# Optimization experiments

Hardware: AMD Instinct MI355X
Metric: run time of the kernel (lower is better)

The kernel has to match this reference:

```python
import jax, jax.numpy as jnp
import numpy as np

N, T, D_MODEL, H, DK = 4, 4096, 1024, 16, 64


def setup_inputs() -> dict:
    key = jax.random.key(0)
    ks = jax.random.split(key, 16)
    randn = lambda k, sh: jax.random.normal(k, sh, dtype=jnp.float32)
    # linear weights stored (in, out) so y = x @ W + b (math-equivalent to torch Linear)
    scale = 1.0 / np.sqrt(D_MODEL)
    return {
        "x_k": randn(ks[0], (N, T, D_MODEL)),
        "x_v": randn(ks[1], (N, T, D_MODEL)),
        "x_q": randn(ks[2], (N, T, D_MODEL)),
        "mask": jnp.ones((N, T), dtype=jnp.int32),
        "Wk": randn(ks[3], (D_MODEL, H * DK)) * scale,
        "bk": randn(ks[4], (H * DK,)) * 0.02,
        "Wv": randn(ks[5], (D_MODEL, H * DK)) * scale,
        "bv": randn(ks[6], (H * DK,)) * 0.02,
        "Wq": randn(ks[7], (D_MODEL, H * DK)) * scale,
        "bq": randn(ks[8], (H * DK,)) * 0.02,
        "alpha_w": randn(ks[9], (DK,)),
        "beta_w": randn(ks[10], (DK,)),
        "Wr": randn(ks[11], (DK, DK)) * (1.0 / np.sqrt(DK)),
        "br": randn(ks[12], (DK,)) * 0.02,
        "Wfc": randn(ks[13], (H * DK, D_MODEL)) * scale,
        "bfc": randn(ks[14], (D_MODEL,)) * 0.02,
    }


def _split_heads(x):  # (n, t, h*d) -> (n, h, t, d)
    n, t, _ = x.shape
    return x.reshape(n, t, H, DK).transpose(0, 2, 1, 3)


def reference(x_k, x_v, x_q, mask, Wk, bk, Wv, bv, Wq, bq,
              alpha_w, beta_w, Wr, br, Wfc, bfc):
    scale = DK ** (-0.5)
    k = _split_heads(x_k @ Wk + bk)  # (n, h, t, d)
    v = _split_heads(x_v @ Wv + bv)
    q = _split_heads(x_q @ Wq + bq)

    m = (mask == 0)[:, None, :]  # (n, 1, t) True where masked
    neg_inf = jnp.finfo(q.dtype).min

    # alpha pooling over queries -> global query (n, h, d)
    alpha = jnp.einsum('nhtd,d->nht', q, alpha_w) * scale
    alpha = jnp.where(m, neg_inf, alpha)
    alpha = jax.nn.softmax(alpha, axis=-1)
    global_query = jnp.einsum('nht,nhtd->nhd', alpha, q)

    # p = broadcast(global_query) * k, then beta pooling -> global key
    p = global_query[:, :, None, :] * k  # (n, h, t, d)
    beta = jnp.einsum('nhtd,d->nht', p, beta_w) * scale
    beta = jnp.where(m, neg_inf, beta)
    beta = jax.nn.softmax(beta, axis=-1)
    global_key = jnp.einsum('nht,nhtd->nhd', beta, p)

    u = global_key[:, :, None, :] * v  # (n, h, t, d)
    u_r = u @ Wr + br
    A = u_r + q  # (n, h, t, d)
    A = A.transpose(0, 2, 1, 3).reshape(N, T, H * DK)
    return A @ Wfc + bfc
```

## Files before the change

kernel.cpp:

```cpp
#include <hip/hip_runtime.h>

typedef __bf16 bf16x8 __attribute__((ext_vector_type(8)));
typedef float f32x4 __attribute__((ext_vector_type(4)));
typedef unsigned int u32x4 __attribute__((ext_vector_type(4)));
typedef unsigned short u16x4 __attribute__((ext_vector_type(4)));
typedef unsigned short u16x8 __attribute__((ext_vector_type(8)));

#define SEQ_T 4096
#define DMODEL 1024
#define HEADS 16
#define DKH 64
#define MTOK 16384

#define AS1 __attribute__((address_space(1)))
#define AS3 __attribute__((address_space(3)))

__device__ __forceinline__ unsigned short f2bf(float f) {
  unsigned u = __builtin_bit_cast(unsigned int, f);
  u += 0x7FFFu + ((u >> 16) & 1u);
  return (unsigned short)(u >> 16);
}
__device__ __forceinline__ float bf2f(unsigned short h) {
  unsigned u = ((unsigned)h) << 16;
  return __builtin_bit_cast(float, u);
}
__device__ __forceinline__ void gload16(const unsigned short* g, unsigned short* l) {
  __builtin_amdgcn_global_load_lds((const AS1 unsigned int*)(g),
                                   (AS3 unsigned int*)(l), 16, 0, 0);
}

__global__ void __launch_bounds__(256) k_wtrans(const float* __restrict__ W,
                                                unsigned short* __restrict__ Wt,
                                                int K, int N) {
  __shared__ float tile[32][33];
  int bn = blockIdx.x * 32, bk = blockIdx.y * 32;
  int tx = threadIdx.x, ty = threadIdx.y;
#pragma unroll
  for (int j = 0; j < 32; j += 8)
    tile[ty + j][tx] = W[(size_t)(bk + ty + j) * N + bn + tx];
  __syncthreads();
#pragma unroll
  for (int j = 0; j < 32; j += 8)
    Wt[(size_t)(bn + ty + j) * K + bk + tx] = f2bf(tile[tx][ty + j]);
}

#define BM 256
#define BN 256
#define BK 64

template <int OBF, int SCORE, int AF32>
__global__ void __launch_bounds__(512, 2)
k_gemm(const void* __restrict__ Ain, const unsigned short* __restrict__ Bt,
       const float* __restrict__ bias, void* __restrict__ C,
       const int* __restrict__ mask, const float* __restrict__ swt,
       float* __restrict__ sbuf, int M, int N, int K) {
  __shared__ unsigned short Asb[2][BM * BK];
  __shared__ unsigned short Bsb[2][BN * BK];
  const int tid = threadIdx.x;
  const int lane = tid & 63, wid = tid >> 6;
  const int wr = wid >> 2, wc = wid & 3;
  const int l15 = lane & 15, l4 = lane >> 4;

  const int nwg = gridDim.x * gridDim.y;
  const int flat = blockIdx.x + blockIdx.y * gridDim.x;
  const int rm = (flat & 7) * (nwg >> 3) + (flat >> 3);
  const int bx = rm % gridDim.x, by = rm / gridDim.x;
  const int bm = by * BM, bn = bx * BN;

  const float* Af = (const float*)Ain;
  const unsigned short* Abf = (const unsigned short*)Ain;

  f32x4 acc[8][4];
#pragma unroll
  for (int i = 0; i < 8; ++i)
#pragma unroll
    for (int j = 0; j < 4; ++j)
#pragma unroll
      for (int e = 0; e < 4; ++e) acc[i][j][e] = 0.f;

  const int sgr = lane >> 3;
  const int sgc = (lane & 7) ^ sgr;
  const int r0 = tid >> 3;
  const int c7l = tid & 7;
  const int c7s = c7l ^ (r0 & 7);

  f32x4 alo[4], ahi[4];
  auto loadA32 = [&](int t) {
#pragma unroll
    for (int s = 0; s < 4; ++s) {
      const float* src = Af + (size_t)(bm + r0 + s * 64) * K + t * BK + c7s * 8;
      alo[s] = *(const f32x4*)src;
      ahi[s] = *(const f32x4*)(src + 4);
    }
  };
  auto writeA32 = [&](int t) {
    unsigned short* dst = &Asb[t & 1][0];
#pragma unroll
    for (int s = 0; s < 4; ++s) {
      u16x8 o;
#pragma unroll
      for (int j = 0; j < 4; ++j) {
        o[j] = f2bf(alo[s][j]);
        o[4 + j] = f2bf(ahi[s][j]);
      }
      *(u16x8*)(dst + (r0 + s * 64) * BK + c7l * 8) = o;
    }
  };
  auto stageAbf = [&](int t) {
    unsigned short* dst = &Asb[t & 1][0];
#pragma unroll
    for (int j = 0; j < 4; ++j) {
      int g = wid * 4 + j;
      gload16(Abf + (size_t)(bm + g * 8 + sgr) * K + t * BK + sgc * 8,
              dst + g * 512);
    }
  };
  auto stageB = [&](int t) {
    unsigned short* dst = &Bsb[t & 1][0];
#pragma unroll
    for (int j = 0; j < 4; ++j) {
      int g = wid * 4 + j;
      gload16(Bt + (size_t)(bn + g * 8 + sgr) * K + t * BK + sgc * 8,
              dst + g * 512);
    }
  };

  const int nt = K / BK;
  if (AF32) {
    loadA32(0);
    writeA32(0);
  } else {
    stageAbf(0);
  }
  stageB(0);

  for (int t = 0; t < nt; ++t) {
    asm volatile("s_waitcnt vmcnt(0)" ::: "memory");
    asm volatile("s_waitcnt lgkmcnt(0)" ::: "memory");
    __builtin_amdgcn_s_barrier();
    const bool pf = (t + 1 < nt);
    if (pf) {
      if (AF32) loadA32(t + 1); else stageAbf(t + 1);
      stageB(t + 1);
    }
    const unsigned short* Ab = &Asb[t & 1][0];
    const unsigned short* Bb = &Bsb[t & 1][0];
#pragma unroll
    for (int ks = 0; ks < 2; ++ks) {
      bf16x8 bfr[4];
#pragma unroll
      for (int nf = 0; nf < 4; ++nf) {
        int rowb = wc * 64 + nf * 16 + l15;
        int c7 = (ks * 4 + l4) ^ (rowb & 7);
        bfr[nf] = *(const bf16x8*)(Bb + rowb * BK + c7 * 8);
      }
#pragma unroll
      for (int mh = 0; mh < 2; ++mh) {
        bf16x8 af[4];
#pragma unroll
        for (int i = 0; i < 4; ++i) {
          int rowa = wr * 128 + (mh * 4 + i) * 16 + l15;
          int c7 = (ks * 4 + l4) ^ (rowa & 7);
          af[i] = *(const bf16x8*)(Ab + rowa * BK + c7 * 8);
        }
        __builtin_amdgcn_s_setprio(1);
#pragma unroll
        for (int i = 0; i < 4; ++i)
#pragma unroll
          for (int nf = 0; nf < 4; ++nf)
            acc[mh * 4 + i][nf] = __builtin_amdgcn_mfma_f32_16x16x32_bf16(
                af[i], bfr[nf], acc[mh * 4 + i][nf], 0, 0, 0);
        __builtin_amdgcn_s_setprio(0);
      }
    }
    if (pf && AF32) writeA32(t + 1);
    asm volatile("s_waitcnt lgkmcnt(0)" ::: "memory");
    __builtin_amdgcn_s_barrier();
  }

  const int crow = bm + wr * 128 + l4 * 4;
  const int ccol = bn + wc * 64 + l15;
  float pacc[8][4];
  const float* wrow = nullptr;
  if (SCORE == 1) wrow = swt;
  if (SCORE == 2)
    wrow = swt + ((size_t)((bm >> 12) * HEADS + bx * 4 + wc)) * DKH;
  if (SCORE) {
#pragma unroll
    for (int m = 0; m < 8; ++m)
#pragma unroll
      for (int e = 0; e < 4; ++e) pacc[m][e] = 0.f;
  }

#pragma unroll
  for (int m = 0; m < 8; ++m)
#pragma unroll
    for (int nf = 0; nf < 4; ++nf) {
      int c = ccol + nf * 16;
      float bj = bias[c];
      float wg = SCORE ? wrow[nf * 16 + l15] : 0.f;
#pragma unroll
      for (int e = 0; e < 4; ++e) {
        int r = crow + m * 16 + e;
        float v = acc[m][nf][e] + bj;
        if (SCORE) pacc[m][e] += v * wg;
        if (OBF)
          ((unsigned short*)C)[(size_t)r * N + c] = f2bf(v);
        else
          ((float*)C)[(size_t)r * N + c] = v;
      }
    }

  if (SCORE) {
#pragma unroll
    for (int m = 0; m < 8; ++m)
#pragma unroll
      for (int e = 0; e < 4; ++e) {
        float p = pacc[m][e];
        p += __shfl_xor(p, 1);
        p += __shfl_xor(p, 2);
        p += __shfl_xor(p, 4);
        p += __shfl_xor(p, 8);
        if (l15 == 0) {
          int r = crow + m * 16 + e;
          int t = r & (SEQ_T - 1), n = r >> 12;
          float sc = p * 0.125f;
          if (mask[n * SEQ_T + t] == 0) sc = -3.0e38f;
          sbuf[((size_t)n * HEADS + bx * 4 + wc) * SEQ_T + t] = sc;
        }
      }
  }
}

__global__ void __launch_bounds__(256) k_stat1(const float* __restrict__ s,
                                               float* __restrict__ pmax,
                                               float* __restrict__ psum) {
  __shared__ float red[4];
  const int b = blockIdx.x, tid = threadIdx.x, lane = tid & 63, wid = tid >> 6;
  float v = s[(size_t)b * 256 + tid];
  float m = v;
#pragma unroll
  for (int o = 1; o < 64; o <<= 1) m = fmaxf(m, __shfl_xor(m, o));
  if (lane == 0) red[wid] = m;
  __syncthreads();
  m = fmaxf(fmaxf(red[0], red[1]), fmaxf(red[2], red[3]));
  __syncthreads();
  float e = __expf(v - m);
#pragma unroll
  for (int o = 1; o < 64; o <<= 1) e += __shfl_xor(e, o);
  if (lane == 0) red[wid] = e;
  __syncthreads();
  if (tid == 0) {
    pmax[b] = m;
    psum[b] = red[0] + red[1] + red[2] + red[3];
  }
}

__global__ void __launch_bounds__(64) k_stat2(const float* __restrict__ pmax,
                                              const float* __restrict__ psum,
                                              float* __restrict__ smx,
                                              float* __restrict__ sinv) {
  const int b = blockIdx.x, lane = threadIdx.x;
  float pm = -3.4e38f, ps = 0.f;
  if (lane < 16) {
    pm = pmax[b * 16 + lane];
    ps = psum[b * 16 + lane];
  }
  float gm = pm;
#pragma unroll
  for (int o = 1; o < 16; o <<= 1) gm = fmaxf(gm, __shfl_xor(gm, o));
  float sc = ps * __expf(pm - gm);
#pragma unroll
  for (int o = 1; o < 16; o <<= 1) sc += __shfl_xor(sc, o);
  if (lane == 0) {
    smx[b] = gm;
    sinv[b] = 1.f / sc;
  }
}

__global__ void __launch_bounds__(256) k_wsum(const unsigned short* __restrict__ X,
                                              const float* __restrict__ s,
                                              const float* __restrict__ mxv,
                                              const float* __restrict__ invv,
                                              float* __restrict__ pbuf) {
  __shared__ float part[16][64];
  const int nh = blockIdx.x >> 4, chunk = blockIdx.x & 15;
  const int n = nh >> 4, h = nh & 15;
  const int tid = threadIdx.x, lane = tid & 63, wid = tid >> 6;
  const int tsub = lane >> 4, dl = lane & 15;
  const float mx = mxv[nh], inv = invv[nh];
  const float* sb = s + (size_t)nh * SEQ_T + chunk * 256;
  const size_t base = ((size_t)n * SEQ_T + chunk * 256) * DMODEL + h * DKH + dl * 4;
  f32x4 acc = {0.f, 0.f, 0.f, 0.f};
  for (int t = wid * 4 + tsub; t < 256; t += 16) {
    float w = __expf(sb[t] - mx) * inv;
    u16x4 xv = *(const u16x4*)(X + base + (size_t)t * DMODEL);
    acc[0] += w * bf2f(xv[0]);
    acc[1] += w * bf2f(xv[1]);
    acc[2] += w * bf2f(xv[2]);
    acc[3] += w * bf2f(xv[3]);
  }
  int g = wid * 4 + tsub;
#pragma unroll
  for (int e = 0; e < 4; ++e) part[g][dl * 4 + e] = acc[e];
  __syncthreads();
  if (tid < 64) {
    float v = 0.f;
#pragma unroll
    for (int gg = 0; gg < 16; ++gg) v += part[gg][tid];
    pbuf[(size_t)blockIdx.x * 64 + tid] = v;
  }
}

template <int MODE>
__global__ void __launch_bounds__(64) k_fin(const float* __restrict__ pbuf,
                                            const float* __restrict__ gq,
                                            const float* __restrict__ bw,
                                            float* __restrict__ out,
                                            float* __restrict__ wv) {
  const int nh = blockIdx.x, d = threadIdx.x;
  float v = 0.f;
#pragma unroll
  for (int c = 0; c < 16; ++c) v += pbuf[((size_t)nh * 16 + c) * 64 + d];
  if (MODE == 1) v *= gq[(size_t)nh * 64 + d];
  out[(size_t)nh * 64 + d] = v;
  if (MODE == 0) wv[(size_t)nh * 64 + d] = v * bw[d];
}

__global__ void __launch_bounds__(256) k_wrg(const float* __restrict__ gk,
                                             const float* __restrict__ Wr,
                                             unsigned short* __restrict__ WrgT) {
  const int nh = blockIdx.x, tid = threadIdx.x;
#pragma unroll
  for (int i = 0; i < 16; ++i) {
    int idx = i * 256 + tid;
    int d = idx >> 6, dd = idx & 63;
    WrgT[(size_t)nh * 4096 + idx] = f2bf(gk[nh * 64 + dd] * Wr[dd * 64 + d]);
  }
}

#define ABM 128
#define VLD 72
__global__ void __launch_bounds__(256) k_abuild2(const unsigned short* __restrict__ v,
                                                 const unsigned short* __restrict__ qbf,
                                                 const unsigned short* __restrict__ WrgT,
                                                 const float* __restrict__ br,
                                                 unsigned short* __restrict__ A) {
  __shared__ unsigned short Vs[ABM * VLD];
  __shared__ unsigned short Ws[DKH * VLD];
  const int tid = threadIdx.x, lane = tid & 63, wid = tid >> 6;
  const int nh = blockIdx.y;
  const int n = nh >> 4, h = nh & 15;
  const size_t nt0 = (size_t)n * SEQ_T + (size_t)blockIdx.x * ABM;
  const size_t vbase = nt0 * DMODEL + (size_t)h * DKH;
#pragma unroll
  for (int p = 0; p < 4; ++p) {
    int idx = p * 256 + tid;
    int row = idx >> 3, c = idx & 7;
    *(u32x4*)(Vs + row * VLD + c * 8) =
        *(const u32x4*)(v + vbase + (size_t)row * DMODEL + c * 8);
  }
#pragma unroll
  for (int p = 0; p < 2; ++p) {
    int idx = p * 256 + tid;
    int row = idx >> 3, c = idx & 7;
    *(u32x4*)(Ws + row * VLD + c * 8) =
        *(const u32x4*)(WrgT + (size_t)nh * 4096 + row * 64 + c * 8);
  }
  __syncthreads();
  const int l15 = lane & 15, l4 = lane >> 4;
  f32x4 acc[2][4];
#pragma unroll
  for (int m = 0; m < 2; ++m)
#pragma unroll
    for (int nf = 0; nf < 4; ++nf)
#pragma unroll
      for (int e = 0; e < 4; ++e) acc[m][nf][e] = 0.f;
#pragma unroll
  for (int ks = 0; ks < 2; ++ks) {
    bf16x8 af[2], bfr[4];
#pragma unroll
    for (int m = 0; m < 2; ++m)
      af[m] = *(const bf16x8*)(Vs + (wid * 32 + m * 16 + l15) * VLD + l4 * 8 + ks * 32);
#pragma unroll
    for (int nf = 0; nf < 4; ++nf)
      bfr[nf] = *(const bf16x8*)(Ws + (nf * 16 + l15) * VLD + l4 * 8 + ks * 32);
#pragma unroll
    for (int m = 0; m < 2; ++m)
#pragma unroll
      for (int nf = 0; nf < 4; ++nf)
        acc[m][nf] = __builtin_amdgcn_mfma_f32_16x16x32_bf16(af[m], bfr[nf],
                                                             acc[m][nf], 0, 0, 0);
  }
#pragma unroll
  for (int m = 0; m < 2; ++m)
#pragma unroll
    for (int nf = 0; nf < 4; ++nf) {
      int d = nf * 16 + l15;
      float bj = br[d];
#pragma unroll
      for (int e = 0; e < 4; ++e) {
        int r = wid * 32 + m * 16 + l4 * 4 + e;
        size_t off = vbase + (size_t)r * DMODEL + d;
        float val = acc[m][nf][e] + bj + bf2f(qbf[off]);
        A[off] = f2bf(val);
      }
    }
}

extern "C" void kernel_launch(void* const* d_in, const int* in_sizes, int n_in,
                              void* d_out, int out_size, void* d_ws, size_t ws_size,
                              hipStream_t stream) {
  const float* x_k = (const float*)d_in[0];
  const float* x_v = (const float*)d_in[1];
  const float* x_q = (const float*)d_in[2];
  const int* mask = (const int*)d_in[3];
  const float* Wk = (const float*)d_in[4];
  const float* bk = (const float*)d_in[5];
  const float* Wv = (const float*)d_in[6];
  const float* bv = (const float*)d_in[7];
  const float* Wq = (const float*)d_in[8];
  const float* bq = (const float*)d_in[9];
  const float* alpha_w = (const float*)d_in[10];
  const float* beta_w = (const float*)d_in[11];
  const float* Wr = (const float*)d_in[12];
  const float* br = (const float*)d_in[13];
  const float* Wfc = (const float*)d_in[14];
  const float* bfc = (const float*)d_in[15];

  unsigned short* qbf = (unsigned short*)d_out;

  char* ws = (char*)d_ws;
  const size_t SZ_XBF = (size_t)MTOK * DMODEL * 2;
  unsigned short* kbf = (unsigned short*)(ws);
  unsigned short* vbf = (unsigned short*)(ws + SZ_XBF);
  unsigned short* xst = (unsigned short*)(ws + 2 * SZ_XBF);
  unsigned short* WkT = (unsigned short*)(ws + 3 * SZ_XBF);
  unsigned short* WvT = WkT + (size_t)DMODEL * DMODEL;
  unsigned short* WqT = WvT + (size_t)DMODEL * DMODEL;
  unsigned short* WfT = WqT + (size_t)DMODEL * DMODEL;
  unsigned short* WrgT = WfT + (size_t)DMODEL * DMODEL;
  float* gq = (float*)(WrgT + (size_t)64 * 4096);
  float* gk = gq + 4096;
  float* wvb = gk + 4096;
  float* sbuf = wvb + 4096;
  float* pbuf = sbuf + (size_t)64 * SEQ_T;
  float* pmax = pbuf + 1024 * 64;
  float* psum = pmax + 1024;
  float* smx = psum + 1024;
  float* sinv = smx + 64;

  dim3 tb(32, 8);
  dim3 tg(DMODEL / 32, DMODEL / 32);
  k_wtrans<<<tg, tb, 0, stream>>>(Wq, WqT, DMODEL, DMODEL);
  k_wtrans<<<tg, tb, 0, stream>>>(Wk, WkT, DMODEL, DMODEL);
  k_wtrans<<<tg, tb, 0, stream>>>(Wv, WvT, DMODEL, DMODEL);
  k_wtrans<<<tg, tb, 0, stream>>>(Wfc, WfT, DMODEL, DMODEL);

  dim3 ggrid(DMODEL / BN, MTOK / BM);

  k_gemm<1, 1, 1><<<ggrid, 512, 0, stream>>>(x_q, WqT, bq, (void*)qbf, mask,
                                             alpha_w, sbuf, MTOK, DMODEL, DMODEL);
  k_stat1<<<1024, 256, 0, stream>>>(sbuf, pmax, psum);
  k_stat2<<<64, 64, 0, stream>>>(pmax, psum, smx, sinv);
  k_wsum<<<1024, 256, 0, stream>>>(qbf, sbuf, smx, sinv, pbuf);
  k_fin<0><<<64, 64, 0, stream>>>(pbuf, nullptr, beta_w, gq, wvb);

  k_gemm<1, 2, 1><<<ggrid, 512, 0, stream>>>(x_k, WkT, bk, (void*)kbf, mask,
                                             wvb, sbuf, MTOK, DMODEL, DMODEL);
  k_stat1<<<1024, 256, 0, stream>>>(sbuf, pmax, psum);
  k_stat2<<<64, 64, 0, stream>>>(pmax, psum, smx, sinv);
  k_wsum<<<1024, 256, 0, stream>>>(kbf, sbuf, smx, sinv, pbuf);
  k_fin<1><<<64, 64, 0, stream>>>(pbuf, gq, nullptr, gk, nullptr);

  k_gemm<1, 0, 1><<<ggrid, 512, 0, stream>>>(x_v, WvT, bv, (void*)vbf, nullptr,
                                             nullptr, nullptr, MTOK, DMODEL, DMODEL);

  k_wrg<<<64, 256, 0, stream>>>(gk, Wr, WrgT);
  dim3 agrid(SEQ_T / ABM, 64);
  k_abuild2<<<agrid, 256, 0, stream>>>(vbf, qbf, WrgT, br, xst);

  k_gemm<0, 0, 0><<<ggrid, 512, 0, stream>>>(xst, WfT, bfc, d_out, nullptr,
                                             nullptr, nullptr, MTOK, DMODEL, DMODEL);
}
```

Before: 297.6 us.

## Restructure GEMM into four-phase pipelined schedule with split half-tile LDS staging

Changes the GEMM main loop so each wave owns a 32-row strip across all 256 columns instead of a 128x64 subtile. LDS A and B tiles are split into 128-row halves, and loads are issued per phase, with B prefetched two k-steps ahead and partial vmcnt waits. Each k-step becomes four barrier-separated MFMA phases, so global-to-LDS transfers overlap compute more finely. The intent is to hide load latency and drop the full vmcnt(0) drain per iteration. The cost is more barriers per k-step and more B-fragment LDS reads per wave, since each wave now reads the whole B tile.

```diff
diff --git a/kernel.cpp b/kernel.cpp
--- a/kernel.cpp
+++ b/kernel.cpp
@@ -14,6 +14,7 @@
 
 #define AS1 __attribute__((address_space(1)))
 #define AS3 __attribute__((address_space(3)))
+#define MEMFENCE asm volatile("" ::: "memory")
 
 __device__ __forceinline__ unsigned short f2bf(float f) {
   unsigned u = __builtin_bit_cast(unsigned int, f);
@@ -54,11 +55,10 @@
        const float* __restrict__ bias, void* __restrict__ C,
        const int* __restrict__ mask, const float* __restrict__ swt,
        float* __restrict__ sbuf, int M, int N, int K) {
-  __shared__ unsigned short Asb[2][BM * BK];
-  __shared__ unsigned short Bsb[2][BN * BK];
+  __shared__ unsigned short As[2][2][128 * 64];
+  __shared__ unsigned short Bs[2][2][128 * 64];
   const int tid = threadIdx.x;
   const int lane = tid & 63, wid = tid >> 6;
-  const int wr = wid >> 2, wc = wid & 3;
   const int l15 = lane & 15, l4 = lane >> 4;
 
   const int nwg = gridDim.x * gridDim.y;
@@ -69,141 +69,172 @@
 
   const float* Af = (const float*)Ain;
   const unsigned short* Abf = (const unsigned short*)Ain;
-
-  f32x4 acc[8][4];
-#pragma unroll
-  for (int i = 0; i < 8; ++i)
-#pragma unroll
-    for (int j = 0; j < 4; ++j)
-#pragma unroll
-      for (int e = 0; e < 4; ++e) acc[i][j][e] = 0.f;
+  const int nt = K / BK;
+
+  f32x4 acc[2][16];
+#pragma unroll
+  for (int m = 0; m < 2; ++m)
+#pragma unroll
+    for (int nf = 0; nf < 16; ++nf)
+#pragma unroll
+      for (int e = 0; e < 4; ++e) acc[m][nf][e] = 0.f;
 
   const int sgr = lane >> 3;
   const int sgc = (lane & 7) ^ sgr;
   const int r0 = tid >> 3;
-  const int c7l = tid & 7;
-  const int c7s = c7l ^ (r0 & 7);
-
+  const int c8 = tid & 7;
+  const int cw = c8 ^ (r0 & 7);
   f32x4 alo[4], ahi[4];
-  auto loadA32 = [&](int t) {
+
+  auto stageA = [&](int t, int h) {
+#pragma unroll
+    for (int j = 0; j < 2; ++j) {
+      int g = wid * 2 + j;
+      gload16(Abf + (size_t)(bm + h * 128 + g * 8 + sgr) * K + t * BK + sgc * 8,
+              &As[t & 1][h][g * 512]);
+    }
+  };
+  auto stageB = [&](int t, int h) {
+#pragma unroll
+    for (int j = 0; j < 2; ++j) {
+      int g = wid * 2 + j;
+      gload16(Bt + (size_t)(bn + h * 128 + g * 8 + sgr) * K + t * BK + sgc * 8,
+              &Bs[t & 1][h][g * 512]);
+    }
+  };
+  auto aload = [&](int t) {
 #pragma unroll
     for (int s = 0; s < 4; ++s) {
-      const float* src = Af + (size_t)(bm + r0 + s * 64) * K + t * BK + c7s * 8;
+      const float* src = Af + (size_t)(bm + r0 + s * 64) * K + t * BK + c8 * 8;
       alo[s] = *(const f32x4*)src;
       ahi[s] = *(const f32x4*)(src + 4);
     }
   };
-  auto writeA32 = [&](int t) {
-    unsigned short* dst = &Asb[t & 1][0];
+  auto awrite = [&](int t) {
 #pragma unroll
     for (int s = 0; s < 4; ++s) {
+      int row = r0 + s * 64;
       u16x8 o;
 #pragma unroll
       for (int j = 0; j < 4; ++j) {
         o[j] = f2bf(alo[s][j]);
         o[4 + j] = f2bf(ahi[s][j]);
       }
-      *(u16x8*)(dst + (r0 + s * 64) * BK + c7l * 8) = o;
+      *(u16x8*)(&As[t & 1][row >> 7][(row & 127) * 64 + cw * 8]) = o;
     }
   };
-  auto stageAbf = [&](int t) {
-    unsigned short* dst = &Asb[t & 1][0];
-#pragma unroll
-    for (int j = 0; j < 4; ++j) {
-      int g = wid * 4 + j;
-      gload16(Abf + (size_t)(bm + g * 8 + sgr) * K + t * BK + sgc * 8,
-              dst + g * 512);
-    }
-  };
-  auto stageB = [&](int t) {
-    unsigned short* dst = &Bsb[t & 1][0];
-#pragma unroll
-    for (int j = 0; j < 4; ++j) {
-      int g = wid * 4 + j;
-      gload16(Bt + (size_t)(bn + g * 8 + sgr) * K + t * BK + sgc * 8,
-              dst + g * 512);
-    }
-  };
-
-  const int nt = K / BK;
+
   if (AF32) {
-    loadA32(0);
-    writeA32(0);
+    aload(0);
+    stageB(0, 0);
+    stageB(0, 1);
+    stageB(1, 0);
+    awrite(0);
+    asm volatile("s_waitcnt lgkmcnt(0)" ::: "memory");
+    asm volatile("s_waitcnt vmcnt(4)" ::: "memory");
   } else {
-    stageAbf(0);
-  }
-  stageB(0);
-
+    stageA(0, 0);
+    stageA(0, 1);
+    stageB(0, 0);
+    stageB(0, 1);
+    stageB(1, 0);
+    asm volatile("s_waitcnt vmcnt(4)" ::: "memory");
+  }
+  __builtin_amdgcn_s_barrier();
+  MEMFENCE;
+
+  bf16x8 afr[2][2];
   for (int t = 0; t < nt; ++t) {
-    asm volatile("s_waitcnt vmcnt(0)" ::: "memory");
-    asm volatile("s_waitcnt lgkmcnt(0)" ::: "memory");
-    __builtin_amdgcn_s_barrier();
-    const bool pf = (t + 1 < nt);
-    if (pf) {
-      if (AF32) loadA32(t + 1); else stageAbf(t + 1);
-      stageB(t + 1);
-    }
-    const unsigned short* Ab = &Asb[t & 1][0];
-    const unsigned short* Bb = &Bsb[t & 1][0];
-#pragma unroll
-    for (int ks = 0; ks < 2; ++ks) {
-      bf16x8 bfr[4];
-#pragma unroll
-      for (int nf = 0; nf < 4; ++nf) {
-        int rowb = wc * 64 + nf * 16 + l15;
-        int c7 = (ks * 4 + l4) ^ (rowb & 7);
-        bfr[nf] = *(const bf16x8*)(Bb + rowb * BK + c7 * 8);
+    const int cur = t & 1;
+#pragma unroll
+    for (int p = 0; p < 4; ++p) {
+      if (p == 0) {
+#pragma unroll
+        for (int m = 0; m < 2; ++m)
+#pragma unroll
+          for (int ks = 0; ks < 2; ++ks) {
+            int rh = (wid & 3) * 32 + m * 16 + l15;
+            int c7 = (ks * 4 + l4) ^ (rh & 7);
+            afr[m][ks] = *(const bf16x8*)(&As[cur][wid >> 2][rh * 64 + c7 * 8]);
+          }
       }
-#pragma unroll
-      for (int mh = 0; mh < 2; ++mh) {
-        bf16x8 af[4];
-#pragma unroll
-        for (int i = 0; i < 4; ++i) {
-          int rowa = wr * 128 + (mh * 4 + i) * 16 + l15;
-          int c7 = (ks * 4 + l4) ^ (rowa & 7);
-          af[i] = *(const bf16x8*)(Ab + rowa * BK + c7 * 8);
+      bf16x8 bfr[4][2];
+#pragma unroll
+      for (int nf = 0; nf < 4; ++nf)
+#pragma unroll
+        for (int ks = 0; ks < 2; ++ks) {
+          int rh = (p & 1) * 64 + nf * 16 + l15;
+          int c7 = (ks * 4 + l4) ^ (rh & 7);
+          bfr[nf][ks] = *(const bf16x8*)(&Bs[cur][p >> 1][rh * 64 + c7 * 8]);
         }
-        __builtin_amdgcn_s_setprio(1);
-#pragma unroll
-        for (int i = 0; i < 4; ++i)
-#pragma unroll
-          for (int nf = 0; nf < 4; ++nf)
-            acc[mh * 4 + i][nf] = __builtin_amdgcn_mfma_f32_16x16x32_bf16(
-                af[i], bfr[nf], acc[mh * 4 + i][nf], 0, 0, 0);
-        __builtin_amdgcn_s_setprio(0);
+      if (p == 0) {
+        if (t + 1 < nt) {
+          if (AF32) aload(t + 1);
+          else stageA(t + 1, 0);
+        }
+      } else if (p == 1) {
+        if (!AF32 && t + 1 < nt) stageA(t + 1, 1);
+      } else if (p == 2) {
+        if (t + 2 < nt) stageB(t + 2, 0);
+      } else {
+        if (t + 1 < nt) {
+          stageB(t + 1, 1);
+          if (AF32) awrite(t + 1);
+        }
       }
-    }
-    if (pf && AF32) writeA32(t + 1);
-    asm volatile("s_waitcnt lgkmcnt(0)" ::: "memory");
-    __builtin_amdgcn_s_barrier();
-  }
-
-  const int crow = bm + wr * 128 + l4 * 4;
-  const int ccol = bn + wc * 64 + l15;
-  float pacc[8][4];
-  const float* wrow = nullptr;
-  if (SCORE == 1) wrow = swt;
-  if (SCORE == 2)
-    wrow = swt + ((size_t)((bm >> 12) * HEADS + bx * 4 + wc)) * DKH;
+      if (p == 1) {
+        if (AF32) asm volatile("s_waitcnt vmcnt(8)" ::: "memory");
+        else asm volatile("s_waitcnt vmcnt(4)" ::: "memory");
+      } else if (p == 3) {
+        if (AF32) asm volatile("s_waitcnt lgkmcnt(0)" ::: "memory");
+        asm volatile("s_waitcnt vmcnt(4)" ::: "memory");
+      }
+      MEMFENCE;
+      __builtin_amdgcn_s_barrier();
+      MEMFENCE;
+      __builtin_amdgcn_s_setprio(1);
+#pragma unroll
+      for (int m = 0; m < 2; ++m)
+#pragma unroll
+        for (int nf = 0; nf < 4; ++nf)
+#pragma unroll
+          for (int ks = 0; ks < 2; ++ks)
+            acc[m][p * 4 + nf] = __builtin_amdgcn_mfma_f32_16x16x32_bf16(
+                afr[m][ks], bfr[nf][ks], acc[m][p * 4 + nf], 0, 0, 0);
+      __builtin_amdgcn_s_setprio(0);
+      MEMFENCE;
+      __builtin_amdgcn_s_barrier();
+      MEMFENCE;
+    }
+  }
+
+  const int crow = bm + wid * 32 + l4 * 4;
+  float pacc[2][4][4];
   if (SCORE) {
 #pragma unroll
-    for (int m = 0; m < 8; ++m)
-#pragma unroll
-      for (int e = 0; e < 4; ++e) pacc[m][e] = 0.f;
-  }
-
-#pragma unroll
-  for (int m = 0; m < 8; ++m)
-#pragma unroll
-    for (int nf = 0; nf < 4; ++nf) {
-      int c = ccol + nf * 16;
+    for (int m = 0; m < 2; ++m)
+#pragma unroll
+      for (int hh = 0; hh < 4; ++hh)
+#pragma unroll
+        for (int e = 0; e < 4; ++e) pacc[m][hh][e] = 0.f;
+  }
+
+#pragma unroll
+  for (int m = 0; m < 2; ++m)
+#pragma unroll
+    for (int nf = 0; nf < 16; ++nf) {
+      int c = bn + nf * 16 + l15;
       float bj = bias[c];
-      float wg = SCORE ? wrow[nf * 16 + l15] : 0.f;
+      float wg = 0.f;
+      if (SCORE == 1) wg = swt[(nf & 3) * 16 + l15];
+      if (SCORE == 2)
+        wg = swt[((size_t)((bm >> 12) * HEADS + bx * 4 + (nf >> 2))) * DKH +
+                 (nf & 3) * 16 + l15];
 #pragma unroll
       for (int e = 0; e < 4; ++e) {
         int r = crow + m * 16 + e;
         float v = acc[m][nf][e] + bj;
-        if (SCORE) pacc[m][e] += v * wg;
+        if (SCORE) pacc[m][nf >> 2][e] += v * wg;
         if (OBF)
           ((unsigned short*)C)[(size_t)r * N + c] = f2bf(v);
         else
@@ -213,22 +244,24 @@
 
   if (SCORE) {
 #pragma unroll
-    for (int m = 0; m < 8; ++m)
-#pragma unroll
-      for (int e = 0; e < 4; ++e) {
-        float p = pacc[m][e];
-        p += __shfl_xor(p, 1);
-        p += __shfl_xor(p, 2);
-        p += __shfl_xor(p, 4);
-        p += __shfl_xor(p, 8);
-        if (l15 == 0) {
-          int r = crow + m * 16 + e;
-          int t = r & (SEQ_T - 1), n = r >> 12;
-          float sc = p * 0.125f;
-          if (mask[n * SEQ_T + t] == 0) sc = -3.0e38f;
-          sbuf[((size_t)n * HEADS + bx * 4 + wc) * SEQ_T + t] = sc;
+    for (int m = 0; m < 2; ++m)
+#pragma unroll
+      for (int hh = 0; hh < 4; ++hh)
+#pragma unroll
+        for (int e = 0; e < 4; ++e) {
+          float pv = pacc[m][hh][e];
+          pv += __shfl_xor(pv, 1);
+          pv += __shfl_xor(pv, 2);
+          pv += __shfl_xor(pv, 4);
+          pv += __shfl_xor(pv, 8);
+          if (l15 == 0) {
+            int r = crow + m * 16 + e;
+            int tt = r & (SEQ_T - 1), n = r >> 12;
+            float sc = pv * 0.125f;
+            if (mask[n * SEQ_T + tt] == 0) sc = -3.0e38f;
+            sbuf[((size_t)n * HEADS + bx * 4 + hh) * SEQ_T + tt] = sc;
+          }
         }
-      }
   }
 }
 
```

Result: no change. 296.3 us (-0.4%).

## Restructure GEMM main loop into an eight-phase interleaved ping-pong schedule

Applied to the files above, without the earlier changes.

The GEMM K-loop is rewritten to process two K tiles per iteration in eight phases. Global-to-LDS staging for the next tiles (A load, B load, fp32 A conversion write, vmcnt wait) is spread across the phases between MFMA bursts, instead of being issued in one block at the top of each tile. Shared buffers are split into 128-row halves, and the fp32-A swizzle moves from the global read side to the LDS write side. The aim is finer overlap of memory traffic with MFMA work, at the cost of two barriers per phase and more synchronization overall.

```diff
diff --git a/kernel.cpp b/kernel.cpp
--- a/kernel.cpp
+++ b/kernel.cpp
@@ -14,6 +14,7 @@
 
 #define AS1 __attribute__((address_space(1)))
 #define AS3 __attribute__((address_space(3)))
+#define MEMFENCE asm volatile("" ::: "memory")
 
 __device__ __forceinline__ unsigned short f2bf(float f) {
   unsigned u = __builtin_bit_cast(unsigned int, f);
@@ -54,8 +55,8 @@
        const float* __restrict__ bias, void* __restrict__ C,
        const int* __restrict__ mask, const float* __restrict__ swt,
        float* __restrict__ sbuf, int M, int N, int K) {
-  __shared__ unsigned short Asb[2][BM * BK];
-  __shared__ unsigned short Bsb[2][BN * BK];
+  __shared__ unsigned short As[2][2][128 * 64];
+  __shared__ unsigned short Bs[2][2][128 * 64];
   const int tid = threadIdx.x;
   const int lane = tid & 63, wid = tid >> 6;
   const int wr = wid >> 2, wc = wid & 3;
@@ -69,128 +70,147 @@
 
   const float* Af = (const float*)Ain;
   const unsigned short* Abf = (const unsigned short*)Ain;
+  const int nt = K / BK;
 
   f32x4 acc[8][4];
 #pragma unroll
-  for (int i = 0; i < 8; ++i)
-#pragma unroll
-    for (int j = 0; j < 4; ++j)
-#pragma unroll
-      for (int e = 0; e < 4; ++e) acc[i][j][e] = 0.f;
+  for (int m = 0; m < 8; ++m)
+#pragma unroll
+    for (int nf = 0; nf < 4; ++nf)
+#pragma unroll
+      for (int e = 0; e < 4; ++e) acc[m][nf][e] = 0.f;
 
   const int sgr = lane >> 3;
   const int sgc = (lane & 7) ^ sgr;
   const int r0 = tid >> 3;
-  const int c7l = tid & 7;
-  const int c7s = c7l ^ (r0 & 7);
-
+  const int c8 = tid & 7;
+  const int cw = c8 ^ (r0 & 7);
   f32x4 alo[4], ahi[4];
-  auto loadA32 = [&](int t) {
+
+  auto stageA = [&](int t) {
+#pragma unroll
+    for (int h = 0; h < 2; ++h)
+#pragma unroll
+      for (int j = 0; j < 2; ++j) {
+        int g = wid * 2 + j;
+        gload16(Abf + (size_t)(bm + h * 128 + g * 8 + sgr) * K + t * BK + sgc * 8,
+                &As[t & 1][h][g * 512]);
+      }
+  };
+  auto stageB = [&](int t) {
+#pragma unroll
+    for (int h = 0; h < 2; ++h)
+#pragma unroll
+      for (int j = 0; j < 2; ++j) {
+        int g = wid * 2 + j;
+        gload16(Bt + (size_t)(bn + h * 128 + g * 8 + sgr) * K + t * BK + sgc * 8,
+                &Bs[t & 1][h][g * 512]);
+      }
+  };
+  auto aload = [&](int t) {
 #pragma unroll
     for (int s = 0; s < 4; ++s) {
-      const float* src = Af + (size_t)(bm + r0 + s * 64) * K + t * BK + c7s * 8;
+      const float* src = Af + (size_t)(bm + r0 + s * 64) * K + t * BK + c8 * 8;
       alo[s] = *(const f32x4*)src;
       ahi[s] = *(const f32x4*)(src + 4);
     }
   };
-  auto writeA32 = [&](int t) {
-    unsigned short* dst = &Asb[t & 1][0];
+  auto awrite = [&](int t) {
 #pragma unroll
     for (int s = 0; s < 4; ++s) {
+      int row = r0 + s * 64;
       u16x8 o;
 #pragma unroll
       for (int j = 0; j < 4; ++j) {
         o[j] = f2bf(alo[s][j]);
         o[4 + j] = f2bf(ahi[s][j]);
       }
-      *(u16x8*)(dst + (r0 + s * 64) * BK + c7l * 8) = o;
+      *(u16x8*)(&As[t & 1][row >> 7][(row & 127) * 64 + cw * 8]) = o;
     }
   };
-  auto stageAbf = [&](int t) {
-    unsigned short* dst = &Asb[t & 1][0];
-#pragma unroll
-    for (int j = 0; j < 4; ++j) {
-      int g = wid * 4 + j;
-      gload16(Abf + (size_t)(bm + g * 8 + sgr) * K + t * BK + sgc * 8,
-              dst + g * 512);
+
+  if (AF32) {
+    aload(0);
+    awrite(0);
+  } else {
+    stageA(0);
+  }
+  stageB(0);
+  asm volatile("s_waitcnt vmcnt(0)" ::: "memory");
+  asm volatile("s_waitcnt lgkmcnt(0)" ::: "memory");
+  __builtin_amdgcn_s_barrier();
+  MEMFENCE;
+
+  bf16x8 bfr[4];
+  for (int it = 0; it < nt / 2; ++it) {
+    const int tA = 2 * it, tB = 2 * it + 1;
+#pragma unroll
+    for (int ph = 0; ph < 8; ++ph) {
+      const int tsel = ph >> 2;
+      const int kh = (ph >> 1) & 1;
+      const int mh = ph & 1;
+      if (mh == 0) {
+#pragma unroll
+        for (int nf = 0; nf < 4; ++nf) {
+          int lr = (wc & 1) * 64 + nf * 16 + l15;
+          int c7 = (kh * 4 + l4) ^ (lr & 7);
+          bfr[nf] = *(const bf16x8*)(&Bs[tsel][wc >> 1][lr * 64 + c7 * 8]);
+        }
+      }
+      bf16x8 af[4];
+#pragma unroll
+      for (int i = 0; i < 4; ++i) {
+        int lr = (mh * 4 + i) * 16 + l15;
+        int c7 = (kh * 4 + l4) ^ (lr & 7);
+        af[i] = *(const bf16x8*)(&As[tsel][wr][lr * 64 + c7 * 8]);
+      }
+      if (ph == 0) {
+        if (AF32) aload(tB); else stageA(tB);
+      } else if (ph == 1) {
+        stageB(tB);
+      } else if (ph == 2) {
+        if (AF32) awrite(tB);
+      } else if (ph == 3) {
+        asm volatile("s_waitcnt vmcnt(0)" ::: "memory");
+      } else if (ph == 4) {
+        if (tA + 2 < nt) { if (AF32) aload(tA + 2); else stageA(tA + 2); }
+      } else if (ph == 5) {
+        if (tA + 2 < nt) stageB(tA + 2);
+      } else if (ph == 6) {
+        if (AF32 && tA + 2 < nt) awrite(tA + 2);
+      } else {
+        asm volatile("s_waitcnt vmcnt(0)" ::: "memory");
+      }
+      MEMFENCE;
+      __builtin_amdgcn_s_barrier();
+      asm volatile("s_waitcnt lgkmcnt(0)" ::: "memory");
+      __builtin_amdgcn_s_setprio(1);
+#pragma unroll
+      for (int i = 0; i < 4; ++i)
+#pragma unroll
+        for (int nf = 0; nf < 4; ++nf)
+          acc[mh * 4 + i][nf] = __builtin_amdgcn_mfma_f32_16x16x32_bf16(
+              af[i], bfr[nf], acc[mh * 4 + i][nf], 0, 0, 0);
+      __builtin_amdgcn_s_setprio(0);
+      MEMFENCE;
+      __builtin_amdgcn_s_barrier();
+      MEMFENCE;
     }
-  };
-  auto stageB = [&](int t) {
-    unsigned short* dst = &Bsb[t & 1][0];
-#pragma unroll
-    for (int j = 0; j < 4; ++j) {
-      int g = wid * 4 + j;
-      gload16(Bt + (size_t)(bn + g * 8 + sgr) * K + t * BK + sgc * 8,
-              dst + g * 512);
-    }
-  };
-
-  const int nt = K / BK;
-  if (AF32) {
-    loadA32(0);
-    writeA32(0);
-  } else {
-    stageAbf(0);
-  }
-  stageB(0);
-
-  for (int t = 0; t < nt; ++t) {
-    asm volatile("s_waitcnt vmcnt(0)" ::: "memory");
-    asm volatile("s_waitcnt lgkmcnt(0)" ::: "memory");
-    __builtin_amdgcn_s_barrier();
-    const bool pf = (t + 1 < nt);
-    if (pf) {
-      if (AF32) loadA32(t + 1); else stageAbf(t + 1);
-      stageB(t + 1);
-    }
-    const unsigned short* Ab = &Asb[t & 1][0];
-    const unsigned short* Bb = &Bsb[t & 1][0];
-#pragma unroll
-    for (int ks = 0; ks < 2; ++ks) {
-      bf16x8 bfr[4];
-#pragma unroll
-      for (int nf = 0; nf < 4; ++nf) {
-        int rowb = wc * 64 + nf * 16 + l15;
-        int c7 = (ks * 4 + l4) ^ (rowb & 7);
-        bfr[nf] = *(const bf16x8*)(Bb + rowb * BK + c7 * 8);
-      }
-#pragma unroll
-      for (int mh = 0; mh < 2; ++mh) {
-        bf16x8 af[4];
-#pragma unroll
-        for (int i = 0; i < 4; ++i) {
-          int rowa = wr * 128 + (mh * 4 + i) * 16 + l15;
-          int c7 = (ks * 4 + l4) ^ (rowa & 7);
-          af[i] = *(const bf16x8*)(Ab + rowa * BK + c7 * 8);
-        }
-        __builtin_amdgcn_s_setprio(1);
-#pragma unroll
-        for (int i = 0; i < 4; ++i)
-#pragma unroll
-          for (int nf = 0; nf < 4; ++nf)
-            acc[mh * 4 + i][nf] = __builtin_amdgcn_mfma_f32_16x16x32_bf16(
-                af[i], bfr[nf], acc[mh * 4 + i][nf], 0, 0, 0);
-        __builtin_amdgcn_s_setprio(0);
-      }
-    }
-    if (pf && AF32) writeA32(t + 1);
-    asm volatile("s_waitcnt lgkmcnt(0)" ::: "memory");
-    __builtin_amdgcn_s_barrier();
   }
 
   const int crow = bm + wr * 128 + l4 * 4;
   const int ccol = bn + wc * 64 + l15;
   float pacc[8][4];
+  if (SCORE) {
+#pragma unroll
+    for (int m = 0; m < 8; ++m)
+#pragma unroll
+      for (int e = 0; e < 4; ++e) pacc[m][e] = 0.f;
+  }
   const float* wrow = nullptr;
   if (SCORE == 1) wrow = swt;
   if (SCORE == 2)
     wrow = swt + ((size_t)((bm >> 12) * HEADS + bx * 4 + wc)) * DKH;
-  if (SCORE) {
-#pragma unroll
-    for (int m = 0; m < 8; ++m)
-#pragma unroll
-      for (int e = 0; e < 4; ++e) pacc[m][e] = 0.f;
-  }
 
 #pragma unroll
   for (int m = 0; m < 8; ++m)
@@ -216,17 +236,17 @@
     for (int m = 0; m < 8; ++m)
 #pragma unroll
       for (int e = 0; e < 4; ++e) {
-        float p = pacc[m][e];
-        p += __shfl_xor(p, 1);
-        p += __shfl_xor(p, 2);
-        p += __shfl_xor(p, 4);
-        p += __shfl_xor(p, 8);
+        float pv = pacc[m][e];
+        pv += __shfl_xor(pv, 1);
+        pv += __shfl_xor(pv, 2);
+        pv += __shfl_xor(pv, 4);
+        pv += __shfl_xor(pv, 8);
         if (l15 == 0) {
           int r = crow + m * 16 + e;
-          int t = r & (SEQ_T - 1), n = r >> 12;
-          float sc = p * 0.125f;
-          if (mask[n * SEQ_T + t] == 0) sc = -3.0e38f;
-          sbuf[((size_t)n * HEADS + bx * 4 + wc) * SEQ_T + t] = sc;
+          int tt = r & (SEQ_T - 1), n = r >> 12;
+          float sc = pv * 0.125f;
+          if (mask[n * SEQ_T + tt] == 0) sc = -3.0e38f;
+          sbuf[((size_t)n * HEADS + bx * 4 + wc) * SEQ_T + tt] = sc;
         }
       }
   }
```

Result: slower. 368.7 us (+23.9%).
